# Optimization experiments

Hardware: AMD Instinct MI355X
Metric: run time of the kernel (lower is better)

## Reference

```python
import jax, jax.numpy as jnp
import numpy as np

B, S, D, H, KVH, HD, NREP = 1, 2048, 5120, 64, 8, 128, 8
CACHE_B, MAX_S = 32, 2048
EPS = 1e-6


def setup_inputs() -> dict:
    key = jax.random.key(0)
    ks = jax.random.split(key, 8)
    x = jax.random.normal(ks[0], (B, S, D), dtype=jnp.float32)
    # torch nn.Linear stores weight as [out_features, in_features]
    wq = jax.random.normal(ks[1], (H * HD, D), dtype=jnp.float32) * 0.02
    wk = jax.random.normal(ks[2], (KVH * HD, D), dtype=jnp.float32) * 0.02
    wv = jax.random.normal(ks[3], (KVH * HD, D), dtype=jnp.float32) * 0.02
    wo = jax.random.normal(ks[4], (D, H * HD), dtype=jnp.float32) * 0.02
    q_norm_w = jnp.ones((HD,), dtype=jnp.float32)
    k_norm_w = jnp.ones((HD,), dtype=jnp.float32)
    cache_k = jnp.zeros((CACHE_B, MAX_S, KVH, HD), dtype=jnp.float32)
    cache_v = jnp.zeros((CACHE_B, MAX_S, KVH, HD), dtype=jnp.float32)
    # rotary frequencies: theta = 10000^{-2i/d}
    inv_freq = 1.0 / (10000.0 ** (jnp.arange(0, HD, 2, dtype=jnp.float32) / HD))  # [64]
    angles = jnp.arange(S, dtype=jnp.float32)[:, None] * inv_freq[None, :]  # [S,64]
    freqs_cos = jnp.cos(angles)
    freqs_sin = jnp.sin(angles)
    # causal additive mask [S, S]
    mask = jnp.triu(jnp.full((S, S), -1e9, dtype=jnp.float32), k=1)
    return {
        "x": x, "wq": wq, "wk": wk, "wv": wv, "wo": wo,
        "q_norm_w": q_norm_w, "k_norm_w": k_norm_w,
        "cache_k": cache_k, "cache_v": cache_v,
        "freqs_cos": freqs_cos, "freqs_sin": freqs_sin,
        "mask": mask, "start_pos": 0,
    }


def _rmsnorm(v, w):
    vf = v.astype(jnp.float32)
    n = vf * jax.lax.rsqrt(jnp.mean(vf * vf, axis=-1, keepdims=True) + EPS)
    return n.astype(v.dtype) * w


def _rope(v, cos, sin):
    # v: [B,S,h,HD]; pairs (even, odd) rotated by angle per pair
    vr = v.reshape(*v.shape[:-1], HD // 2, 2)
    ve, vo = vr[..., 0], vr[..., 1]
    cos = cos[None, :, None, :]  # [1,S,1,64]
    sin = sin[None, :, None, :]
    oe = ve * cos - vo * sin
    oo = ve * sin + vo * cos
    return jnp.stack([oe, oo], axis=-1).reshape(v.shape)


def reference(x, wq, wk, wv, wo, q_norm_w, k_norm_w, cache_k, cache_v,
              freqs_cos, freqs_sin, mask, start_pos):
    bsz, seqlen, _ = x.shape
    xq = (x @ wq.T).reshape(bsz, seqlen, H, HD)
    xk = (x @ wk.T).reshape(bsz, seqlen, KVH, HD)
    xv = (x @ wv.T).reshape(bsz, seqlen, KVH, HD)
    xq = _rmsnorm(xq, q_norm_w)
    xk = _rmsnorm(xk, k_norm_w)
    xq = _rope(xq, freqs_cos, freqs_sin)
    xk = _rope(xk, freqs_cos, freqs_sin)
    # KV-cache append
    cache_k = jax.lax.dynamic_update_slice(cache_k, xk, (0, start_pos, 0, 0))
    cache_v = jax.lax.dynamic_update_slice(cache_v, xv, (0, start_pos, 0, 0))
    kv_len = start_pos + seqlen
    keys = cache_k[:bsz, :kv_len]    # [B,T,KVH,HD]
    values = cache_v[:bsz, :kv_len]
    # GQA expansion (repeat_interleave over kv heads)
    keys = jnp.repeat(keys, NREP, axis=2)      # [B,T,H,HD]
    values = jnp.repeat(values, NREP, axis=2)
    scores = jnp.einsum('bqhd,bkhd->bhqk', xq, keys) / np.float32(np.sqrt(HD))
    if mask is not None:
        scores = scores + mask[None, None, :, :]
    probs = jax.nn.softmax(scores.astype(jnp.float32), axis=-1).astype(xq.dtype)
    out = jnp.einsum('bhqk,bkhd->bqhd', probs, values)
    out = out.reshape(bsz, seqlen, H * HD)
    return out @ wo.T
```

## Files before the change

kernel.cpp:

```cpp
#include <hip/hip_runtime.h>

typedef unsigned short ushort_t;
typedef __attribute__((ext_vector_type(8))) short short8;
typedef __attribute__((ext_vector_type(4))) float f32x4;
typedef __attribute__((ext_vector_type(16))) float f32x16;

#define AS1U(p) ((const __attribute__((address_space(1))) unsigned int*)(p))
#define AS3U(p) ((__attribute__((address_space(3))) unsigned int*)(p))

__device__ __forceinline__ float bf2f(ushort_t u) {
  union { unsigned int i; float f; } v; v.i = ((unsigned int)u) << 16; return v.f;
}
__device__ __forceinline__ ushort_t f2bf(float f) {
  union { float f; unsigned int i; } v; v.f = f;
  unsigned int r = v.i + 0x7fffu + ((v.i >> 16) & 1u);
  return (ushort_t)(r >> 16);
}

template <int N>
__device__ __forceinline__ void waitvm() {
  if constexpr (N == 0) asm volatile("s_waitcnt vmcnt(0)" ::: "memory");
  else if constexpr (N == 2) asm volatile("s_waitcnt vmcnt(2)" ::: "memory");
  else if constexpr (N == 4) asm volatile("s_waitcnt vmcnt(4)" ::: "memory");
  else if constexpr (N == 5) asm volatile("s_waitcnt vmcnt(5)" ::: "memory");
  else if constexpr (N == 8) asm volatile("s_waitcnt vmcnt(8)" ::: "memory");
  else if constexpr (N == 10) asm volatile("s_waitcnt vmcnt(10)" ::: "memory");
}

#define PACK8(dst, S, base)                                                             \
  {                                                                                     \
    union { unsigned int u[4]; short8 s; } pk;                                          \
    asm("v_cvt_pk_bf16_f32 %0, %1, %2" : "=v"(pk.u[0]) : "v"(S[base + 0]), "v"(S[base + 1])); \
    asm("v_cvt_pk_bf16_f32 %0, %1, %2" : "=v"(pk.u[1]) : "v"(S[base + 2]), "v"(S[base + 3])); \
    asm("v_cvt_pk_bf16_f32 %0, %1, %2" : "=v"(pk.u[2]) : "v"(S[base + 4]), "v"(S[base + 5])); \
    asm("v_cvt_pk_bf16_f32 %0, %1, %2" : "=v"(pk.u[3]) : "v"(S[base + 6]), "v"(S[base + 7])); \
    dst = pk.s;                                                                         \
  }

__global__ void cvt_bf16(const float* __restrict__ src, ushort_t* __restrict__ dst, int n8) {
  int i = blockIdx.x * 256 + threadIdx.x;
  if (i >= n8) return;
  const float4* s4 = (const float4*)src;
  float4 a = s4[2 * i], b = s4[2 * i + 1];
  short8 u;
  u[0] = (short)f2bf(a.x); u[1] = (short)f2bf(a.y); u[2] = (short)f2bf(a.z); u[3] = (short)f2bf(a.w);
  u[4] = (short)f2bf(b.x); u[5] = (short)f2bf(b.y); u[6] = (short)f2bf(b.z); u[7] = (short)f2bf(b.w);
  *(short8*)(dst + (size_t)i * 8) = u;
}

template <int OUTF32, int MF, int NF>
__global__ __launch_bounds__(512, 2) void gemmQ(const ushort_t* __restrict__ A,
                                                const ushort_t* __restrict__ B,
                                                void* __restrict__ Cv,
                                                int M, int N, int K) {
  constexpr int BM = MF * 32, BN = NF * 64;
  constexpr int LA = BM / 64, LB = BN / 64;
  constexpr int LMAX = (LA > LB) ? LA : LB;
  constexpr int ABUF = BM * 32;
  __shared__ __align__(16) ushort_t SH[4][(BM + BN) * 32];
  const int t = threadIdx.x;
  const int lane = t & 63, w = t >> 6;
  const int wm = w >> 2, wn = w & 3;
  const int r = lane & 15, g = lane >> 4;
  const int nwg = gridDim.x * gridDim.y;
  const int l = blockIdx.y * gridDim.x + blockIdx.x;
  const int wg = (l & 7) * (nwg >> 3) + (l >> 3);
  const int m0 = (wg & (gridDim.x - 1)) * BM, n0 = (wg / gridDim.x) * BN;
  const int NT = K >> 5;
  const int t256 = t & 255;

  const ushort_t* sp[LMAX];
  int sdst[LMAX];
  if (w < 4) {
#pragma unroll
    for (int i = 0; i < LA; ++i) {
      int s = t256 + i * 256;
      int row = s >> 2, c = s & 3;
      int csrc = c ^ ((row >> 1) & 3);
      sp[i] = A + (size_t)(m0 + row) * K + csrc * 8;
      sdst[i] = s * 8;
    }
  } else {
#pragma unroll
    for (int i = 0; i < LB; ++i) {
      int s = t256 + i * 256;
      int row = s >> 2, c = s & 3;
      int csrc = c ^ ((row >> 1) & 3);
      sp[i] = B + (size_t)(n0 + row) * K + csrc * 8;
      sdst[i] = ABUF + s * 8;
    }
  }
  auto STAGE = [&](int b) {
    if (w < 4) {
#pragma unroll
      for (int i = 0; i < LA; ++i) {
        __builtin_amdgcn_global_load_lds(AS1U(sp[i]), AS3U(&SH[b][0] + sdst[i]), 16, 0, 0);
        sp[i] += 32;
      }
    } else {
#pragma unroll
      for (int i = 0; i < LB; ++i) {
        __builtin_amdgcn_global_load_lds(AS1U(sp[i]), AS3U(&SH[b][0] + sdst[i]), 16, 0, 0);
        sp[i] += 32;
      }
    }
  };

  STAGE(0); STAGE(1); STAGE(2);
  if (w < 4) waitvm<2 * LA>(); else waitvm<2 * LB>();
  __builtin_amdgcn_s_barrier();

  f32x4 acc[MF][NF] = {};
  int bsel = 0;
  const int NI = NT >> 1;
  for (int ii = 0; ii < NI; ++ii) {
    const int s3 = 2 * ii + 3, s4 = 2 * ii + 4;
    const ushort_t* As0 = &SH[bsel][0];
    const ushort_t* Bs0 = &SH[bsel][ABUF];
    const int b1 = (bsel + 1) & 3;
    const ushort_t* As1 = &SH[b1][0];
    const ushort_t* Bs1 = &SH[b1][ABUF];
    short8 bf[NF], af0[MF / 2], af1[MF / 2];

#pragma unroll
    for (int m = 0; m < MF / 2; ++m) {
      int row = wm * (MF * 16) + m * 16 + r;
      af0[m] = *(const short8*)(As0 + row * 32 + (g ^ ((row >> 1) & 3)) * 8);
    }
#pragma unroll
    for (int n = 0; n < NF; ++n) {
      int row = wn * (NF * 16) + n * 16 + r;
      bf[n] = *(const short8*)(Bs0 + row * 32 + (g ^ ((row >> 1) & 3)) * 8);
    }
    if (s3 < NT) STAGE((bsel + 3) & 3);
    __builtin_amdgcn_s_setprio(1);
#pragma unroll
    for (int m = 0; m < MF / 2; ++m)
#pragma unroll
      for (int n = 0; n < NF; ++n)
        acc[m][n] = __builtin_amdgcn_mfma_f32_16x16x32_bf16(af0[m], bf[n], acc[m][n], 0, 0, 0);
    __builtin_amdgcn_s_setprio(0);

#pragma unroll
    for (int m = 0; m < MF / 2; ++m) {
      int row = wm * (MF * 16) + (MF / 2 + m) * 16 + r;
      af1[m] = *(const short8*)(As0 + row * 32 + (g ^ ((row >> 1) & 3)) * 8);
    }
    __builtin_amdgcn_s_setprio(1);
#pragma unroll
    for (int m = 0; m < MF / 2; ++m)
#pragma unroll
      for (int n = 0; n < NF; ++n)
        acc[MF / 2 + m][n] = __builtin_amdgcn_mfma_f32_16x16x32_bf16(af1[m], bf[n], acc[MF / 2 + m][n], 0, 0, 0);
    __builtin_amdgcn_s_setprio(0);
    if (s3 < NT) {
      if (w < 4) waitvm<2 * LA>(); else waitvm<2 * LB>();
    } else if (2 * ii + 2 < NT) {
      if (w < 4) waitvm<LA>(); else waitvm<LB>();
    } else {
      waitvm<0>();
    }
    __builtin_amdgcn_s_barrier();

#pragma unroll
    for (int m = 0; m < MF / 2; ++m) {
      int row = wm * (MF * 16) + m * 16 + r;
      af0[m] = *(const short8*)(As1 + row * 32 + (g ^ ((row >> 1) & 3)) * 8);
    }
#pragma unroll
    for (int n = 0; n < NF; ++n) {
      int row = wn * (NF * 16) + n * 16 + r;
      bf[n] = *(const short8*)(Bs1 + row * 32 + (g ^ ((row >> 1) & 3)) * 8);
    }
    if (s4 < NT) STAGE(bsel);
    __builtin_amdgcn_s_setprio(1);
#pragma unroll
    for (int m = 0; m < MF / 2; ++m)
#pragma unroll
      for (int n = 0; n < NF; ++n)
        acc[m][n] = __builtin_amdgcn_mfma_f32_16x16x32_bf16(af0[m], bf[n], acc[m][n], 0, 0, 0);
    __builtin_amdgcn_s_setprio(0);

#pragma unroll
    for (int m = 0; m < MF / 2; ++m) {
      int row = wm * (MF * 16) + (MF / 2 + m) * 16 + r;
      af1[m] = *(const short8*)(As1 + row * 32 + (g ^ ((row >> 1) & 3)) * 8);
    }
    __builtin_amdgcn_s_setprio(1);
#pragma unroll
    for (int m = 0; m < MF / 2; ++m)
#pragma unroll
      for (int n = 0; n < NF; ++n)
        acc[MF / 2 + m][n] = __builtin_amdgcn_mfma_f32_16x16x32_bf16(af1[m], bf[n], acc[MF / 2 + m][n], 0, 0, 0);
    __builtin_amdgcn_s_setprio(0);
    if (s4 < NT) {
      if (w < 4) waitvm<2 * LA>(); else waitvm<2 * LB>();
    } else if (s3 < NT) {
      if (w < 4) waitvm<LA>(); else waitvm<LB>();
    } else {
      waitvm<0>();
    }
    __builtin_amdgcn_s_barrier();
    bsel = (bsel + 2) & 3;
  }

#pragma unroll
  for (int m = 0; m < MF; ++m)
#pragma unroll
    for (int n = 0; n < NF; ++n)
#pragma unroll
      for (int j = 0; j < 4; ++j) {
        int row = m0 + wm * (MF * 16) + m * 16 + g * 4 + j;
        int col = n0 + wn * (NF * 16) + n * 16 + r;
        if (OUTF32)
          ((float*)Cv)[(size_t)row * N + col] = acc[m][n][j];
        else
          ((ushort_t*)Cv)[(size_t)row * N + col] = f2bf(acc[m][n][j]);
      }
}

__global__ __launch_bounds__(256) void normrope(const ushort_t* __restrict__ qkv,
                                                const float* __restrict__ qw, const float* __restrict__ kw,
                                                const float* __restrict__ fc, const float* __restrict__ fs,
                                                ushort_t* __restrict__ Qb, ushort_t* __restrict__ Kb) {
  const int slot = blockIdx.x * 4 + (threadIdx.x >> 6);
  const int s = blockIdx.y, t = threadIdx.x & 63;
  const ushort_t* src;
  ushort_t* dst;
  const float* wn;
  float scale = 1.0f;
  if (slot < 64) {
    src = qkv + (size_t)s * 10240 + slot * 128;
    dst = Qb + ((size_t)slot * 2048 + s) * 128;
    wn = qw;
    scale = 0.08838834764831845f;
  } else {
    int kh = slot - 64;
    src = qkv + (size_t)s * 10240 + 8192 + kh * 128;
    dst = Kb + ((size_t)kh * 2048 + s) * 128;
    wn = kw;
  }
  float e0 = bf2f(src[2 * t]), e1 = bf2f(src[2 * t + 1]);
  float ss = e0 * e0 + e1 * e1;
#pragma unroll
  for (int m = 1; m < 64; m <<= 1) ss += __shfl_xor(ss, m);
  float rn = rsqrtf(ss * (1.0f / 128.0f) + 1e-6f);
  float v0 = e0 * rn * wn[2 * t], v1 = e1 * rn * wn[2 * t + 1];
  float c = fc[s * 64 + t], sn = fs[s * 64 + t];
  float oe = v0 * c - v1 * sn;
  float oo = v0 * sn + v1 * c;
  dst[2 * t] = f2bf(oe * scale);
  dst[2 * t + 1] = f2bf(oo * scale);
}

__global__ __launch_bounds__(256) void vtrans(const ushort_t* __restrict__ qkv,
                                              ushort_t* __restrict__ Vt) {
  __shared__ __align__(16) ushort_t T[64 * 128];
  const int t = threadIdx.x, st = blockIdx.x, kvh = blockIdx.y;
#pragma unroll
  for (int i = 0; i < 4; ++i) {
    int slot = t + i * 256;
    int srow = slot >> 4, c8 = slot & 15;
    short8 v = *(const short8*)(qkv + (size_t)(st * 64 + srow) * 10240 + 9216 + kvh * 128 + c8 * 8);
    int sw = (((srow & 7) ^ ((srow >> 3) & 7)) << 4);
    *(short8*)((char*)T + srow * 256 + ((c8 * 16) ^ sw)) = v;
  }
  __syncthreads();
#pragma unroll
  for (int i = 0; i < 4; ++i) {
    int slot = t + i * 256;
    int d = slot >> 3, s8 = slot & 7;
    short8 u;
#pragma unroll
    for (int j = 0; j < 8; ++j) {
      int row = s8 * 8 + j;
      int sw = (((row & 7) ^ ((row >> 3) & 7)) << 4);
      u[j] = *(const ushort_t*)((char*)T + row * 256 + ((d * 2) ^ sw));
    }
    *(short8*)(Vt + ((size_t)kvh * 128 + d) * 2048 + st * 64 + s8 * 8) = u;
  }
}

__global__ __launch_bounds__(256) void attn_fwd(const ushort_t* __restrict__ Qg,
                                                const ushort_t* __restrict__ Kg,
                                                const ushort_t* __restrict__ VtG,
                                                ushort_t* __restrict__ Og) {
  __shared__ __align__(16) ushort_t Ks[2][64 * 128];
  __shared__ __align__(16) ushort_t Vs[2][128 * 64];
  const int t = threadIdx.x, lane = t & 63, w = t >> 6;
  const int q5 = lane & 31, hi = lane >> 5;
  const int lb = blockIdx.x;
  const int kvh = lb & 7;
  const int h = kvh * 8 + ((lb >> 3) & 7);
  const int qt = 15 - (lb >> 6);
  const int qrow0 = qt * 128 + w * 32;
  const int qglob = qrow0 + q5;

  const int pa = q5 & 3, pp = (q5 >> 2) & 1, pb = q5 >> 3;
  const int kr = (pb >> 1) * 16 + pp * 8 + (pb & 1) * 4 + pa;
  const int kswz = (kr & 7) << 4;
  const int swz = (q5 & 7) << 4;

  short8 qf[8];
#pragma unroll
  for (int ks = 0; ks < 8; ++ks)
    qf[ks] = *(const short8*)(Qg + ((size_t)h * 2048 + qglob) * 128 + ks * 16 + hi * 8);

  f32x16 o[4] = {};
  float mrun = -3.0e38f, lrun = 0.0f;

  const int kbmax_blk = 2 * qt + 1;
  const int kbmax_w = (qrow0 + 31) >> 6;

  auto STAGE = [&](int b, int kb) {
#pragma unroll
    for (int i = 0; i < 4; ++i) {
      int slot = t + i * 256;
      int kv = slot >> 4, c = slot & 15;
      int csrc = c ^ (kv & 7);
      __builtin_amdgcn_global_load_lds(AS1U(Kg + ((size_t)kvh * 2048 + kb * 64 + kv) * 128 + csrc * 8),
                                       AS3U(&Ks[b][0] + slot * 8), 16, 0, 0);
    }
#pragma unroll
    for (int i = 0; i < 4; ++i) {
      int slot = t + i * 256;
      int d = slot >> 3, c = slot & 7;
      int csrc = c ^ (d & 7);
      __builtin_amdgcn_global_load_lds(AS1U(VtG + ((size_t)kvh * 128 + d) * 2048 + kb * 64 + csrc * 8),
                                       AS3U(&Vs[b][0] + slot * 8), 16, 0, 0);
    }
  };

  STAGE(0, 0);
  int cur = 0;

  for (int kb = 0; kb <= kbmax_blk; ++kb) {
    asm volatile("s_waitcnt vmcnt(0)" ::: "memory");
    __syncthreads();
    if (kb < kbmax_blk) STAGE(cur ^ 1, kb + 1);

    if (kb <= kbmax_w) {
      const char* kbase = (const char*)&Ks[cur][0];
      const char* vbase = (const char*)&Vs[cur][0];

      f32x16 st0 = {}, st1 = {};
#pragma unroll
      for (int ks = 0; ks < 8; ++ks) {
        int cslot = ((ks * 2 + hi) * 16) ^ kswz;
        short8 kf0 = *(const short8*)(kbase + kr * 256 + cslot);
        short8 kf1 = *(const short8*)(kbase + (32 + kr) * 256 + cslot);
        __builtin_amdgcn_s_setprio(1);
        st0 = __builtin_amdgcn_mfma_f32_32x32x16_bf16(kf0, qf[ks], st0, 0, 0, 0);
        st1 = __builtin_amdgcn_mfma_f32_32x32x16_bf16(kf1, qf[ks], st1, 0, 0, 0);
        __builtin_amdgcn_s_setprio(0);
      }

      if (kb == kbmax_w) {
#pragma unroll
        for (int r = 0; r < 16; ++r) {
          int kv0 = kb * 64 + (r >> 3) * 16 + hi * 8 + (r & 7);
          if (kv0 > qglob) st0[r] = -1.0e30f;
          if (kv0 + 32 > qglob) st1[r] = -1.0e30f;
        }
      }

      float pmax = st0[0];
#pragma unroll
      for (int r = 1; r < 16; ++r) pmax = fmaxf(pmax, st0[r]);
#pragma unroll
      for (int r = 0; r < 16; ++r) pmax = fmaxf(pmax, st1[r]);
      pmax = fmaxf(pmax, __shfl_xor(pmax, 32));
      if (!__all(pmax <= mrun + 8.0f)) {
        float mn = fmaxf(mrun, pmax);
        float sc = __expf(mrun - mn);
        mrun = mn;
        lrun *= sc;
#pragma unroll
        for (int db = 0; db < 4; ++db) o[db] *= sc;
      }
      float rs = 0.0f;
#pragma unroll
      for (int r = 0; r < 16; ++r) { st0[r] = __expf(st0[r] - mrun); rs += st0[r]; }
#pragma unroll
      for (int r = 0; r < 16; ++r) { st1[r] = __expf(st1[r] - mrun); rs += st1[r]; }
      rs += __shfl_xor(rs, 32);
      lrun += rs;

      short8 pf[4];
      PACK8(pf[0], st0, 0);
      PACK8(pf[1], st0, 8);
      PACK8(pf[2], st1, 0);
      PACK8(pf[3], st1, 8);

#pragma unroll
      for (int db = 0; db < 4; ++db) {
#pragma unroll
        for (int ks = 0; ks < 4; ++ks) {
          short8 vf = *(const short8*)(vbase + (db * 32 + q5) * 128 + ((((ks * 2 + hi) * 16)) ^ swz));
          __builtin_amdgcn_s_setprio(1);
          o[db] = __builtin_amdgcn_mfma_f32_32x32x16_bf16(vf, pf[ks], o[db], 0, 0, 0);
          __builtin_amdgcn_s_setprio(0);
        }
      }
    }
    cur ^= 1;
  }

  __syncthreads();
  char* tr = ((char*)Ks) + w * 8192;
  float inv = 1.0f / lrun;
#pragma unroll
  for (int db = 0; db < 4; ++db)
#pragma unroll
    for (int r = 0; r < 16; r += 2) {
      unsigned int u;
      float lo = o[db][r] * inv, hiv = o[db][r + 1] * inv;
      asm("v_cvt_pk_bf16_f32 %0, %1, %2" : "=v"(u) : "v"(lo), "v"(hiv));
      int d = db * 32 + (r & 3) + 8 * (r >> 2) + 4 * hi;
      *(unsigned int*)(tr + q5 * 256 + ((d * 2) ^ swz)) = u;
    }
  asm volatile("s_waitcnt lgkmcnt(0)" ::: "memory");
#pragma unroll
  for (int p = 0; p < 8; ++p) {
    int row = (lane >> 3) + (p >> 1) * 8;
    int c = (lane & 7) + (p & 1) * 8;
    short8 v = *(const short8*)(tr + row * 256 + ((c * 16) ^ ((row & 7) << 4)));
    *(short8*)(Og + (size_t)(qrow0 + row) * 8192 + h * 128 + c * 8) = v;
  }
}

extern "C" void kernel_launch(void* const* d_in, const int* in_sizes, int n_in,
                              void* d_out, int out_size, void* d_ws, size_t ws_size,
                              hipStream_t stream) {
  const float* x = (const float*)d_in[0];
  const float* wq = (const float*)d_in[1];
  const float* wk = (const float*)d_in[2];
  const float* wv = (const float*)d_in[3];
  const float* wo = (const float*)d_in[4];
  const float* qw = (const float*)d_in[5];
  const float* kw = (const float*)d_in[6];
  const float* fc = (const float*)d_in[9];
  const float* fs = (const float*)d_in[10];

  char* ws = (char*)d_ws;
  ushort_t* Wb = (ushort_t*)(ws);
  ushort_t* qkv = (ushort_t*)(ws + 104857600);
  ushort_t* xb = (ushort_t*)(ws + 146800640);
  ushort_t* Qb = xb;
  ushort_t* Kb = (ushort_t*)(ws + 180355072);
  ushort_t* Vtb = (ushort_t*)(ws + 184549376);
  ushort_t* attnb = qkv;

  {
    int n8 = 2048 * 5120 / 8;
    cvt_bf16<<<dim3((n8 + 255) / 256), 256, 0, stream>>>(x, xb, n8);
  }
  {
    int n8 = 8192 * 5120 / 8;
    cvt_bf16<<<dim3((n8 + 255) / 256), 256, 0, stream>>>(wq, Wb, n8);
  }
  {
    int n8 = 1024 * 5120 / 8;
    cvt_bf16<<<dim3((n8 + 255) / 256), 256, 0, stream>>>(wk, Wb + (size_t)8192 * 5120, n8);
    cvt_bf16<<<dim3((n8 + 255) / 256), 256, 0, stream>>>(wv, Wb + (size_t)9216 * 5120, n8);
  }

  gemmQ<0, 8, 5><<<dim3(8, 32), 512, 0, stream>>>(xb, Wb, qkv, 2048, 10240, 5120);

  {
    int n8 = 5120 * 8192 / 8;
    cvt_bf16<<<dim3((n8 + 255) / 256), 256, 0, stream>>>(wo, Wb, n8);
  }

  normrope<<<dim3(18, 2048), 256, 0, stream>>>(qkv, qw, kw, fc, fs, Qb, Kb);

  vtrans<<<dim3(32, 8), 256, 0, stream>>>(qkv, Vtb);

  attn_fwd<<<dim3(1024), 256, 0, stream>>>(Qb, Kb, Vtb, attnb);

  gemmQ<1, 4, 5><<<dim3(16, 16), 512, 0, stream>>>(attnb, Wb, (float*)d_out, 2048, 5120, 8192);
}
```

Baseline: 628.9 us.

## Use five-stage LDS ring with one barrier per two k-steps, fuse bf16 converts

The GEMM's shared-memory ring grows from four to five stages, so both half-iterations of the unrolled k-loop run back to back with a single wait and barrier per pair of k-steps instead of one per step. The QKV projection tile shrinks from 256x320 to 128x320 with twice as many blocks, and the four separate fp32-to-bf16 conversion launches for x, wq, wk and wv are merged into one kernel. The goal is fewer barriers and launches and more blocks in flight, at the cost of extra LDS per block, which may reduce occupancy, and modulo-5 buffer index arithmetic.

```diff
diff --git a/kernel.cpp b/kernel.cpp
--- a/kernel.cpp
+++ b/kernel.cpp
@@ -36,6 +36,25 @@
     asm("v_cvt_pk_bf16_f32 %0, %1, %2" : "=v"(pk.u[3]) : "v"(S[base + 6]), "v"(S[base + 7])); \
     dst = pk.s;                                                                         \
   }
+
+__global__ void cvt_all(const float* __restrict__ x, const float* __restrict__ wq,
+                        const float* __restrict__ wk, const float* __restrict__ wv,
+                        ushort_t* __restrict__ xb, ushort_t* __restrict__ Wb) {
+  int i = blockIdx.x * 256 + threadIdx.x;
+  const float* src;
+  ushort_t* dst;
+  int idx;
+  if (i < 1310720) { src = x; dst = xb; idx = i; }
+  else if (i < 6553600) { src = wq; dst = Wb; idx = i - 1310720; }
+  else if (i < 7208960) { src = wk; dst = Wb + 41943040; idx = i - 6553600; }
+  else { src = wv; dst = Wb + 47185920; idx = i - 7208960; }
+  const float4* s4 = (const float4*)(src + (size_t)idx * 8);
+  float4 a = s4[0], b = s4[1];
+  short8 u;
+  u[0] = (short)f2bf(a.x); u[1] = (short)f2bf(a.y); u[2] = (short)f2bf(a.z); u[3] = (short)f2bf(a.w);
+  u[4] = (short)f2bf(b.x); u[5] = (short)f2bf(b.y); u[6] = (short)f2bf(b.z); u[7] = (short)f2bf(b.w);
+  *(short8*)(dst + (size_t)idx * 8) = u;
+}
 
 __global__ void cvt_bf16(const float* __restrict__ src, ushort_t* __restrict__ dst, int n8) {
   int i = blockIdx.x * 256 + threadIdx.x;
@@ -49,7 +68,7 @@
 }
 
 template <int OUTF32, int MF, int NF>
-__global__ __launch_bounds__(512, 2) void gemmQ(const ushort_t* __restrict__ A,
+__global__ __launch_bounds__(512, 2) void gemmR(const ushort_t* __restrict__ A,
                                                 const ushort_t* __restrict__ B,
                                                 void* __restrict__ Cv,
                                                 int M, int N, int K) {
@@ -57,7 +76,7 @@
   constexpr int LA = BM / 64, LB = BN / 64;
   constexpr int LMAX = (LA > LB) ? LA : LB;
   constexpr int ABUF = BM * 32;
-  __shared__ __align__(16) ushort_t SH[4][(BM + BN) * 32];
+  __shared__ __align__(16) ushort_t SH[5][(BM + BN) * 32];
   const int t = threadIdx.x;
   const int lane = t & 63, w = t >> 6;
   const int wm = w >> 2, wn = w & 3;
@@ -107,7 +126,7 @@
   };
 
   STAGE(0); STAGE(1); STAGE(2);
-  if (w < 4) waitvm<2 * LA>(); else waitvm<2 * LB>();
+  if (w < 4) waitvm<LA>(); else waitvm<LB>();
   __builtin_amdgcn_s_barrier();
 
   f32x4 acc[MF][NF] = {};
@@ -115,9 +134,11 @@
   const int NI = NT >> 1;
   for (int ii = 0; ii < NI; ++ii) {
     const int s3 = 2 * ii + 3, s4 = 2 * ii + 4;
+    int b1 = bsel + 1; if (b1 >= 5) b1 -= 5;
+    int b3 = bsel + 3; if (b3 >= 5) b3 -= 5;
+    int b4 = bsel + 4; if (b4 >= 5) b4 -= 5;
     const ushort_t* As0 = &SH[bsel][0];
     const ushort_t* Bs0 = &SH[bsel][ABUF];
-    const int b1 = (bsel + 1) & 3;
     const ushort_t* As1 = &SH[b1][0];
     const ushort_t* Bs1 = &SH[b1][ABUF];
     short8 bf[NF], af0[MF / 2], af1[MF / 2];
@@ -132,7 +153,7 @@
       int row = wn * (NF * 16) + n * 16 + r;
       bf[n] = *(const short8*)(Bs0 + row * 32 + (g ^ ((row >> 1) & 3)) * 8);
     }
-    if (s3 < NT) STAGE((bsel + 3) & 3);
+    if (s3 < NT) STAGE(b3);
     __builtin_amdgcn_s_setprio(1);
 #pragma unroll
     for (int m = 0; m < MF / 2; ++m)
@@ -153,55 +174,46 @@
       for (int n = 0; n < NF; ++n)
         acc[MF / 2 + m][n] = __builtin_amdgcn_mfma_f32_16x16x32_bf16(af1[m], bf[n], acc[MF / 2 + m][n], 0, 0, 0);
     __builtin_amdgcn_s_setprio(0);
-    if (s3 < NT) {
-      if (w < 4) waitvm<2 * LA>(); else waitvm<2 * LB>();
-    } else if (2 * ii + 2 < NT) {
+
+#pragma unroll
+    for (int m = 0; m < MF / 2; ++m) {
+      int row = wm * (MF * 16) + m * 16 + r;
+      af0[m] = *(const short8*)(As1 + row * 32 + (g ^ ((row >> 1) & 3)) * 8);
+    }
+#pragma unroll
+    for (int n = 0; n < NF; ++n) {
+      int row = wn * (NF * 16) + n * 16 + r;
+      bf[n] = *(const short8*)(Bs1 + row * 32 + (g ^ ((row >> 1) & 3)) * 8);
+    }
+    if (s4 < NT) STAGE(b4);
+    __builtin_amdgcn_s_setprio(1);
+#pragma unroll
+    for (int m = 0; m < MF / 2; ++m)
+#pragma unroll
+      for (int n = 0; n < NF; ++n)
+        acc[m][n] = __builtin_amdgcn_mfma_f32_16x16x32_bf16(af0[m], bf[n], acc[m][n], 0, 0, 0);
+    __builtin_amdgcn_s_setprio(0);
+
+#pragma unroll
+    for (int m = 0; m < MF / 2; ++m) {
+      int row = wm * (MF * 16) + (MF / 2 + m) * 16 + r;
+      af1[m] = *(const short8*)(As1 + row * 32 + (g ^ ((row >> 1) & 3)) * 8);
+    }
+    __builtin_amdgcn_s_setprio(1);
+#pragma unroll
+    for (int m = 0; m < MF / 2; ++m)
+#pragma unroll
+      for (int n = 0; n < NF; ++n)
+        acc[MF / 2 + m][n] = __builtin_amdgcn_mfma_f32_16x16x32_bf16(af1[m], bf[n], acc[MF / 2 + m][n], 0, 0, 0);
+    __builtin_amdgcn_s_setprio(0);
+
+    if (s4 < NT) {
       if (w < 4) waitvm<LA>(); else waitvm<LB>();
     } else {
       waitvm<0>();
     }
     __builtin_amdgcn_s_barrier();
-
-#pragma unroll
-    for (int m = 0; m < MF / 2; ++m) {
-      int row = wm * (MF * 16) + m * 16 + r;
-      af0[m] = *(const short8*)(As1 + row * 32 + (g ^ ((row >> 1) & 3)) * 8);
-    }
-#pragma unroll
-    for (int n = 0; n < NF; ++n) {
-      int row = wn * (NF * 16) + n * 16 + r;
-      bf[n] = *(const short8*)(Bs1 + row * 32 + (g ^ ((row >> 1) & 3)) * 8);
-    }
-    if (s4 < NT) STAGE(bsel);
-    __builtin_amdgcn_s_setprio(1);
-#pragma unroll
-    for (int m = 0; m < MF / 2; ++m)
-#pragma unroll
-      for (int n = 0; n < NF; ++n)
-        acc[m][n] = __builtin_amdgcn_mfma_f32_16x16x32_bf16(af0[m], bf[n], acc[m][n], 0, 0, 0);
-    __builtin_amdgcn_s_setprio(0);
-
-#pragma unroll
-    for (int m = 0; m < MF / 2; ++m) {
-      int row = wm * (MF * 16) + (MF / 2 + m) * 16 + r;
-      af1[m] = *(const short8*)(As1 + row * 32 + (g ^ ((row >> 1) & 3)) * 8);
-    }
-    __builtin_amdgcn_s_setprio(1);
-#pragma unroll
-    for (int m = 0; m < MF / 2; ++m)
-#pragma unroll
-      for (int n = 0; n < NF; ++n)
-        acc[MF / 2 + m][n] = __builtin_amdgcn_mfma_f32_16x16x32_bf16(af1[m], bf[n], acc[MF / 2 + m][n], 0, 0, 0);
-    __builtin_amdgcn_s_setprio(0);
-    if (s4 < NT) {
-      if (w < 4) waitvm<2 * LA>(); else waitvm<2 * LB>();
-    } else if (s3 < NT) {
-      if (w < 4) waitvm<LA>(); else waitvm<LB>();
-    } else {
-      waitvm<0>();
-    }
-    __builtin_amdgcn_s_barrier();
-    bsel = (bsel + 2) & 3;
+    bsel += 2; if (bsel >= 5) bsel -= 5;
   }
 
 #pragma unroll
@@ -451,21 +463,9 @@
   ushort_t* Vtb = (ushort_t*)(ws + 184549376);
   ushort_t* attnb = qkv;
 
-  {
-    int n8 = 2048 * 5120 / 8;
-    cvt_bf16<<<dim3((n8 + 255) / 256), 256, 0, stream>>>(x, xb, n8);
-  }
-  {
-    int n8 = 8192 * 5120 / 8;
-    cvt_bf16<<<dim3((n8 + 255) / 256), 256, 0, stream>>>(wq, Wb, n8);
-  }
-  {
-    int n8 = 1024 * 5120 / 8;
-    cvt_bf16<<<dim3((n8 + 255) / 256), 256, 0, stream>>>(wk, Wb + (size_t)8192 * 5120, n8);
-    cvt_bf16<<<dim3((n8 + 255) / 256), 256, 0, stream>>>(wv, Wb + (size_t)9216 * 5120, n8);
-  }
-
-  gemmQ<0, 8, 5><<<dim3(8, 32), 512, 0, stream>>>(xb, Wb, qkv, 2048, 10240, 5120);
+  cvt_all<<<dim3(30720), 256, 0, stream>>>(x, wq, wk, wv, xb, Wb);
+
+  gemmR<0, 4, 5><<<dim3(16, 32), 512, 0, stream>>>(xb, Wb, qkv, 2048, 10240, 5120);
 
   {
     int n8 = 5120 * 8192 / 8;
@@ -478,5 +478,5 @@
 
   attn_fwd<<<dim3(1024), 256, 0, stream>>>(Qb, Kb, Vtb, attnb);
 
-  gemmQ<1, 4, 5><<<dim3(16, 16), 512, 0, stream>>>(attnb, Wb, (float*)d_out, 2048, 5120, 8192);
-}
+  gemmR<1, 4, 5><<<dim3(16, 16), 512, 0, stream>>>(attnb, Wb, (float*)d_out, 2048, 5120, 8192);
+}
```

Result: slower. 649.9 us (+3.3%).
